# Kernel optimization log

Measured on AMD Instinct MI355X. Metric: run time of the kernel, lower is better.

## Reference

```python
import jax, jax.numpy as jnp
import numpy as np

DECAY = 0.99
LR = 0.01

def setup_inputs() -> dict:
    key = jax.random.key(0)
    ks = jax.random.split(key, 6)
    B, S, D, M = 4, 4096, 1024, 128
    sD = 1.0 / np.sqrt(D)
    sM = 1.0 / np.sqrt(M)
    return {
        "x": jax.random.normal(ks[0], (B, S, D), dtype=jnp.float32),
        "Wk": jax.random.uniform(ks[1], (M, D), jnp.float32, -sD, sD),
        "bk": jnp.zeros((M,), jnp.float32),
        "Wv": jax.random.uniform(ks[2], (M, D), jnp.float32, -sD, sD),
        "bv": jnp.zeros((M,), jnp.float32),
        "Wq": jax.random.uniform(ks[3], (M, D), jnp.float32, -sD, sD),
        "bq": jnp.zeros((M,), jnp.float32),
        "Wo": jax.random.uniform(ks[4], (D, M), jnp.float32, -sM, sM),
        "bo": jnp.zeros((D,), jnp.float32),
    }

def reference(x, Wk, bk, Wv, bv, Wq, bq, Wo, bo):
    B, S, D = x.shape
    M = Wk.shape[0]
    # Precompute all projections in one batched GEMM each: [B,S,M]
    k = jnp.einsum('bsd,md->bsm', x, Wk) + bk
    v = jnp.einsum('bsd,md->bsm', x, Wv) + bv
    q = jnp.einsum('bsd,md->bsm', x, Wq) + bq

    def step(state, kvq):
        k_t, v_t, q_t = kvq  # each [B, M]
        # readout uses the PRE-update state, matching the torch loop order
        out_t = jnp.einsum('bij,bj->bi', state, q_t)          # [B, M]
        state = DECAY * state + LR * jnp.einsum('bi,bj->bij', v_t, k_t)
        return state, out_t

    state0 = jnp.zeros((B, M, M), x.dtype)
    # scan over time: move seq axis to front -> [S, B, M]
    xs = (jnp.swapaxes(k, 0, 1), jnp.swapaxes(v, 0, 1), jnp.swapaxes(q, 0, 1))
    state, outs = jax.lax.scan(step, state0, xs)
    outs = jnp.swapaxes(outs, 0, 1)                            # [B, S, M]
    y = jnp.einsum('bsm,dm->bsd', outs, Wo) + bo               # [B, S, D]
    return (y, state)
```

## Files before the change

kernel.cpp:

```cpp
#include <hip/hip_runtime.h>
#include <math.h>

namespace {
constexpr int kB = 4;
constexpr int kS = 4096;
constexpr int kD = 1024;
constexpr int kM = 128;
constexpr int kC = 64;
constexpr int kNC = kS / kC;
constexpr int kNCG = kB * kNC;
constexpr int kRS = kB * kS;
constexpr float kLR = 0.01f;
constexpr float kLog2d = -0.0144995696f;
}

typedef __bf16 bf16x8 __attribute__((ext_vector_type(8)));
typedef float  f32x4  __attribute__((ext_vector_type(4)));
typedef unsigned short u16;
typedef unsigned int   u32;

#define SB0() __builtin_amdgcn_sched_barrier(0)
#define WAITV(N) asm volatile("s_waitcnt vmcnt(" #N ") lgkmcnt(0)" ::: "memory")

__device__ __forceinline__ u16 f2bf(float f) {
  u32 x = __float_as_uint(f);
  u32 r = (x + 0x7fffu + ((x >> 16) & 1u)) >> 16;
  return (u16)r;
}

__device__ __forceinline__ float bf2f(u16 h) {
  return __uint_as_float(((u32)h) << 16);
}

__device__ __forceinline__ void gl_lds16(const void* g, void* l) {
  __builtin_amdgcn_global_load_lds(
      (const __attribute__((address_space(1))) void*)g,
      (__attribute__((address_space(3))) void*)l, 16, 0, 0);
}

__device__ __forceinline__ f32x4 mf(bf16x8 a, bf16x8 b, f32x4 c) {
  return __builtin_amdgcn_mfma_f32_16x16x32_bf16(a, b, c, 0, 0, 0);
}

__device__ __forceinline__ ushort4 pack4(float4 a) {
  ushort4 o;
  o.x = f2bf(a.x); o.y = f2bf(a.y); o.z = f2bf(a.z); o.w = f2bf(a.w);
  return o;
}

__device__ __forceinline__ int fo64x128(int r, int c) {
  return ((r >> 4) * 4 + (c >> 5)) * 1024 + ((c >> 3) & 3) * 256 + (r & 15) * 16 + (c & 7) * 2;
}
__device__ __forceinline__ int fo128x64(int r, int c) {
  return ((r >> 4) * 2 + (c >> 5)) * 1024 + ((c >> 3) & 3) * 256 + (r & 15) * 16 + (c & 7) * 2;
}
__device__ __forceinline__ int fo64x64(int r, int c) {
  return ((r >> 4) * 2 + (c >> 5)) * 1024 + ((c >> 3) & 3) * 256 + (r & 15) * 16 + (c & 7) * 2;
}

__global__ __launch_bounds__(256)
void cast_w_kernel(const float* __restrict__ Wk, const float* __restrict__ Wv,
                   const float* __restrict__ Wq, const float* __restrict__ Wo,
                   u16* __restrict__ Wkvq, u16* __restrict__ Woh)
{
  int i = (blockIdx.x * 256 + threadIdx.x) * 4;
  const float* src;
  u16* dst;
  if (i < 393216) {
    src = (i < 131072) ? Wk + i : (i < 262144) ? Wv + (i - 131072) : Wq + (i - 262144);
    dst = Wkvq + i;
  } else {
    src = Wo + (i - 393216);
    dst = Woh + (i - 393216);
  }
  float4 v = *(const float4*)src;
  *(ushort4*)dst = pack4(v);
}

__global__ __launch_bounds__(256, 2)
void proj_gemm(const float* __restrict__ x, const u16* __restrict__ Wkvq,
               const float* __restrict__ bk, const float* __restrict__ bv,
               const float* __restrict__ bq,
               u16* __restrict__ Qg, u16* __restrict__ Kg,
               u16* __restrict__ VTg, u16* __restrict__ KwTg)
{
  __shared__ __align__(16) u16 L[36864];
  const int cg = blockIdx.x, s = blockIdx.y;
  const int R0 = cg * 64;
  const int tid = threadIdx.x, w = tid >> 6, lane = tid & 63;
  const int fr = lane & 15, qd = lane >> 4;
  const int wr = w >> 1, wc = w & 1;

  const int xr = tid >> 2, s4 = tid & 3;
  const float* xp = x + (size_t)(R0 + xr) * kD + s4 * 4;
  int aoffq[4];
#pragma unroll
  for (int q = 0; q < 4; ++q)
    aoffq[q] = ((xr >> 4) * 2 + (q >> 1)) * 1024 + (((s4 >> 1) + 2 * q) & 3) * 256
             + (xr & 15) * 16 + (s4 & 1) * 8;

  const u16* wbase = Wkvq + (size_t)(128 * s) * kD + qd * 8;

  f32x4 acc[2][4] = {};
  float4 xv0[4], xv1[4];

  auto compute = [&](int cs) {
    bf16x8 af[2][2], bfr2[2][4];
#pragma unroll
    for (int kh = 0; kh < 2; ++kh) {
#pragma unroll
      for (int mi = 0; mi < 2; ++mi)
        af[kh][mi] = *(const bf16x8*)&L[(cs * 8192 + ((wr * 2 + mi) * 2 + kh) * 1024 + qd * 256 + fr * 16) >> 1];
#pragma unroll
      for (int ng = 0; ng < 4; ++ng)
        bfr2[kh][ng] = *(const bf16x8*)&L[(24576 + cs * 16384 + ((wc * 4 + ng) * 2 + kh) * 1024 + qd * 256 + fr * 16) >> 1];
    }
#pragma unroll
    for (int kh = 0; kh < 2; ++kh)
#pragma unroll
      for (int mi = 0; mi < 2; ++mi)
#pragma unroll
        for (int ng = 0; ng < 4; ++ng)
          acc[mi][ng] = mf(af[kh][mi], bfr2[kh][ng], acc[mi][ng]);
  };

  auto step = [&](int t, float4 (&xw)[4], float4 (&xl)[4]) {
    const int wslot = (t + 1) % 3, ns = (t + 2) % 3;
#pragma unroll
    for (int q = 0; q < 4; ++q)
      *(ushort4*)&L[(wslot * 8192 + aoffq[q]) >> 1] = pack4(xw[q]);
    const int k2 = (t + 2) * 64;
#pragma unroll
    for (int g = 0; g < 4; ++g) {
      const int pn = 4 * w + g, ng = pn >> 1, kh = pn & 1;
      gl_lds16(wbase + (size_t)(ng * 16 + fr) * kD + k2 + kh * 32,
               &L[(24576 + ns * 16384 + pn * 1024) >> 1]);
    }
#pragma unroll
    for (int q = 0; q < 4; ++q) xl[q] = *(const float4*)(xp + k2 + q * 16);
    compute(t % 3);
    WAITV(8); SB0(); __builtin_amdgcn_s_barrier(); SB0();
  };

#pragma unroll
  for (int g = 0; g < 4; ++g) {
    const int pn = 4 * w + g, ng = pn >> 1, kh = pn & 1;
    gl_lds16(wbase + (size_t)(ng * 16 + fr) * kD + kh * 32, &L[(24576 + pn * 1024) >> 1]);
  }
#pragma unroll
  for (int q = 0; q < 4; ++q) xv0[q] = *(const float4*)(xp + q * 16);
#pragma unroll
  for (int q = 0; q < 4; ++q) *(ushort4*)&L[(0 + aoffq[q]) >> 1] = pack4(xv0[q]);
#pragma unroll
  for (int g = 0; g < 4; ++g) {
    const int pn = 4 * w + g, ng = pn >> 1, kh = pn & 1;
    gl_lds16(wbase + (size_t)(ng * 16 + fr) * kD + 64 + kh * 32,
             &L[(24576 + 16384 + pn * 1024) >> 1]);
  }
#pragma unroll
  for (int q = 0; q < 4; ++q) xv1[q] = *(const float4*)(xp + 64 + q * 16);
  WAITV(8); SB0(); __builtin_amdgcn_s_barrier(); SB0();

  for (int it = 0; it < 7; ++it) {
    step(2 * it, xv1, xv0);
    step(2 * it + 1, xv0, xv1);
  }
  {
#pragma unroll
    for (int q = 0; q < 4; ++q)
      *(ushort4*)&L[(0 + aoffq[q]) >> 1] = pack4(xv1[q]);
    compute(2);
    WAITV(0); SB0(); __builtin_amdgcn_s_barrier(); SB0();
  }
  compute(0);

  const float* bp = (s == 0) ? bk : (s == 1) ? bv : bq;
  float bias[4];
#pragma unroll
  for (int ng = 0; ng < 4; ++ng) bias[ng] = bp[wc * 64 + ng * 16 + fr];
  const size_t cb = (size_t)cg * 8192;

  if (s == 0) {
    float dp[2][4];
#pragma unroll
    for (int mi = 0; mi < 2; ++mi)
#pragma unroll
      for (int r = 0; r < 4; ++r)
        dp[mi][r] = kLR * exp2f((float)(63 - (wr * 32 + mi * 16 + qd * 4 + r)) * kLog2d);
#pragma unroll
    for (int mi = 0; mi < 2; ++mi)
#pragma unroll
      for (int ng = 0; ng < 4; ++ng)
#pragma unroll
        for (int r = 0; r < 4; ++r) {
          const int t = wr * 32 + mi * 16 + qd * 4 + r, n = wc * 64 + ng * 16 + fr;
          const float v = acc[mi][ng][r] + bias[ng];
          Kg[cb + (fo64x128(t, n) >> 1)] = f2bf(v);
          KwTg[cb + (fo128x64(n, t) >> 1)] = f2bf(v * dp[mi][r]);
        }
  } else if (s == 1) {
#pragma unroll
    for (int mi = 0; mi < 2; ++mi)
#pragma unroll
      for (int ng = 0; ng < 4; ++ng)
#pragma unroll
        for (int r = 0; r < 4; ++r) {
          const int t = wr * 32 + mi * 16 + qd * 4 + r, n = wc * 64 + ng * 16 + fr;
          VTg[cb + (fo128x64(n, t) >> 1)] = f2bf(acc[mi][ng][r] + bias[ng]);
        }
  } else {
#pragma unroll
    for (int mi = 0; mi < 2; ++mi)
#pragma unroll
      for (int ng = 0; ng < 4; ++ng)
#pragma unroll
        for (int r = 0; r < 4; ++r) {
          const int t = wr * 32 + mi * 16 + qd * 4 + r, n = wc * 64 + ng * 16 + fr;
          Qg[cb + (fo64x128(t, n) >> 1)] = f2bf(acc[mi][ng][r] + bias[ng]);
        }
  }
}

__global__ __launch_bounds__(256, 2)
void intra_kernel(const u16* __restrict__ Qg, const u16* __restrict__ Kg,
                  const u16* __restrict__ VTg, const u16* __restrict__ KwTg,
                  u16* __restrict__ O1g, float* __restrict__ SU)
{
  __shared__ __align__(16) u16 L[32768];
  const int cg = blockIdx.x;
  const int tid = threadIdx.x, w = tid >> 6, lane = tid & 63;
  const int fr = lane & 15, qd = lane >> 4;
  const size_t cb = (size_t)cg * 8192;

#pragma unroll
  for (int g = 0; g < 4; ++g) {
    const int pn = 4 * w + g;
    gl_lds16(Qg + cb + pn * 512 + lane * 8, &L[(0 + pn * 1024) >> 1]);
    gl_lds16(Kg + cb + pn * 512 + lane * 8, &L[(16384 + pn * 1024) >> 1]);
    gl_lds16(VTg + cb + pn * 512 + lane * 8, &L[(32768 + pn * 1024) >> 1]);
    gl_lds16(KwTg + cb + pn * 512 + lane * 8, &L[(49152 + pn * 1024) >> 1]);
  }
  __syncthreads();

  f32x4 p[4] = {};
#pragma unroll
  for (int kc = 0; kc < 4; ++kc) {
    bf16x8 aq = *(const bf16x8*)&L[(0 + (w * 4 + kc) * 1024 + qd * 256 + fr * 16) >> 1];
#pragma unroll
    for (int ug = 0; ug < 4; ++ug) {
      bf16x8 bkf = *(const bf16x8*)&L[(16384 + (ug * 4 + kc) * 1024 + qd * 256 + fr * 16) >> 1];
      p[ug] = mf(aq, bkf, p[ug]);
    }
  }
  __syncthreads();

#pragma unroll
  for (int ug = 0; ug < 4; ++ug)
#pragma unroll
    for (int r = 0; r < 4; ++r) {
      const int t = w * 16 + qd * 4 + r, u = ug * 16 + fr;
      float av = 0.f;
      if (u < t) av = kLR * exp2f((float)(t - 1 - u) * kLog2d) * p[ug][r];
      L[(0 + fo64x64(t, u)) >> 1] = f2bf(av);
    }
  __syncthreads();

  f32x4 o1[8] = {}, uu[2][8] = {};
#pragma unroll
  for (int h = 0; h < 2; ++h) {
    bf16x8 aA = *(const bf16x8*)&L[(0 + (w * 2 + h) * 1024 + qd * 256 + fr * 16) >> 1];
    bf16x8 aV[2];
#pragma unroll
    for (int mi = 0; mi < 2; ++mi)
      aV[mi] = *(const bf16x8*)&L[(32768 + ((2 * w + mi) * 2 + h) * 1024 + qd * 256 + fr * 16) >> 1];
#pragma unroll
    for (int ig = 0; ig < 8; ++ig) {
      bf16x8 bV = *(const bf16x8*)&L[(32768 + (ig * 2 + h) * 1024 + qd * 256 + fr * 16) >> 1];
      o1[ig] = mf(aA, bV, o1[ig]);
    }
#pragma unroll
    for (int jg = 0; jg < 8; ++jg) {
      bf16x8 bK = *(const bf16x8*)&L[(49152 + (jg * 2 + h) * 1024 + qd * 256 + fr * 16) >> 1];
#pragma unroll
      for (int mi = 0; mi < 2; ++mi)
        uu[mi][jg] = mf(aV[mi], bK, uu[mi][jg]);
    }
  }

#pragma unroll
  for (int ig = 0; ig < 8; ++ig)
#pragma unroll
    for (int r = 0; r < 4; ++r) {
      const int t = w * 16 + qd * 4 + r, i2 = ig * 16 + fr;
      O1g[cb + (fo64x128(t, i2) >> 1)] = f2bf(o1[ig][r]);
    }
  float* SUc = SU + (size_t)cg * 16384;
#pragma unroll
  for (int mi = 0; mi < 2; ++mi)
#pragma unroll
    for (int jg = 0; jg < 8; ++jg)
#pragma unroll
      for (int r = 0; r < 4; ++r) {
        const int i2 = w * 32 + mi * 16 + qd * 4 + r, j = jg * 16 + fr;
        SUc[i2 * kM + j] = uu[mi][jg][r];
      }
}

__global__ __launch_bounds__(256)
void scan_kernel(const float* __restrict__ SU, u16* __restrict__ Sb16,
                 float* __restrict__ state_out)
{
  const int e = blockIdx.x * 256 + threadIdx.x;
  const int b = e >> 14, ij = e & 16383;
  const float* base = SU + (size_t)b * kNC * 16384 + ij;
  u16* sb = Sb16 + (size_t)b * kNC * 16384 + ij;
  const float dC = exp2f((float)kC * kLog2d);
  float prev = 0.f;
#pragma unroll 8
  for (int c2 = 0; c2 < kNC; ++c2) {
    const float u = base[(size_t)c2 * 16384];
    sb[(size_t)c2 * 16384] = f2bf(prev);
    prev = fmaf(dC, prev, u);
  }
  state_out[e] = prev;
}

__global__ __launch_bounds__(256)
void fused_combine_out(const u16* __restrict__ Qg, const u16* __restrict__ Sb16,
                       const u16* __restrict__ O1g, const u16* __restrict__ Woh,
                       const float* __restrict__ bo, float* __restrict__ y)
{
  __shared__ __align__(16) u16 L[32768];
  const int cg = blockIdx.x;
  const int R0 = cg * 64;
  const int tid = threadIdx.x, w = tid >> 6, lane = tid & 63;
  const int fr = lane & 15, qd = lane >> 4;
  const size_t cb = (size_t)cg * 8192;
  const u16* Sbc = Sb16 + (size_t)cg * 16384;

#pragma unroll
  for (int g = 0; g < 4; ++g) {
    const int pn = 4 * w + g;
    gl_lds16(Qg + cb + pn * 512 + lane * 8, &L[(0 + pn * 1024) >> 1]);
    gl_lds16(O1g + cb + pn * 512 + lane * 8, &L[(49152 + pn * 1024) >> 1]);
  }
#pragma unroll
  for (int g = 0; g < 8; ++g) {
    const int pn = 8 * w + g, ig = pn >> 2, kc = pn & 3;
    gl_lds16(Sbc + (size_t)(ig * 16 + fr) * kM + kc * 32 + qd * 8,
             &L[(16384 + pn * 1024) >> 1]);
  }
  __syncthreads();

  f32x4 o2[8] = {};
#pragma unroll
  for (int kc = 0; kc < 4; ++kc) {
    bf16x8 aq = *(const bf16x8*)&L[(0 + (w * 4 + kc) * 1024 + qd * 256 + fr * 16) >> 1];
#pragma unroll
    for (int ig = 0; ig < 8; ++ig) {
      bf16x8 bS = *(const bf16x8*)&L[(16384 + (ig * 4 + kc) * 1024 + qd * 256 + fr * 16) >> 1];
      o2[ig] = mf(aq, bS, o2[ig]);
    }
  }

  float dt[4];
#pragma unroll
  for (int r = 0; r < 4; ++r) dt[r] = exp2f((float)(w * 16 + qd * 4 + r) * kLog2d);
#pragma unroll
  for (int ig = 0; ig < 8; ++ig)
#pragma unroll
    for (int r = 0; r < 4; ++r) {
      const int t = w * 16 + qd * 4 + r, i2 = ig * 16 + fr;
      const float o1v = bf2f(L[(49152 + fo64x128(t, i2)) >> 1]);
      L[(0 + fo64x128(t, i2)) >> 1] = f2bf(fmaf(dt[r], o2[ig][r], o1v));
    }
  __syncthreads();

#pragma unroll 1
  for (int h = 0; h < 2; ++h) {
    const int n0 = w * 256 + h * 128;
    f32x4 fy[4][8] = {};
#pragma unroll
    for (int kp = 0; kp < 4; ++kp) {
      bf16x8 ao[4], bw[8];
#pragma unroll
      for (int mi = 0; mi < 4; ++mi)
        ao[mi] = *(const bf16x8*)&L[((mi * 4 + kp) * 1024 + qd * 256 + fr * 16) >> 1];
#pragma unroll
      for (int nj = 0; nj < 8; ++nj)
        bw[nj] = *(const bf16x8*)&Woh[(size_t)(n0 + nj * 16 + fr) * kM + kp * 32 + qd * 8];
#pragma unroll
      for (int mi = 0; mi < 4; ++mi)
#pragma unroll
        for (int nj = 0; nj < 8; ++nj)
          fy[mi][nj] = mf(ao[mi], bw[nj], fy[mi][nj]);
    }
#pragma unroll
    for (int nj = 0; nj < 8; ++nj) {
      const int d = n0 + nj * 16 + fr;
      const float bb = bo[d];
#pragma unroll
      for (int mi = 0; mi < 4; ++mi)
#pragma unroll
        for (int r = 0; r < 4; ++r)
          y[(size_t)(R0 + mi * 16 + qd * 4 + r) * kD + d] = fy[mi][nj][r] + bb;
    }
  }
}

extern "C" void kernel_launch(void* const* d_in, const int* in_sizes, int n_in,
                              void* d_out, int out_size, void* d_ws, size_t ws_size,
                              hipStream_t stream) {
  const float* x  = (const float*)d_in[0];
  const float* Wk = (const float*)d_in[1];
  const float* bk = (const float*)d_in[2];
  const float* Wv = (const float*)d_in[3];
  const float* bv = (const float*)d_in[4];
  const float* Wq = (const float*)d_in[5];
  const float* bq = (const float*)d_in[6];
  const float* Wo = (const float*)d_in[7];
  const float* bo = (const float*)d_in[8];

  char* wsp = (char*)d_ws;
  u16* Wkvq = (u16*)wsp;  wsp += (size_t)384 * 1024 * 2;
  u16* Woh  = (u16*)wsp;  wsp += (size_t)1024 * 128 * 2;
  u16* Qg   = (u16*)wsp;  wsp += (size_t)kNCG * 8192 * 2;
  u16* Kg   = (u16*)wsp;  wsp += (size_t)kNCG * 8192 * 2;
  u16* VTg  = (u16*)wsp;
  u16* KwTg = VTg + (size_t)kNCG * 8192;
  u16* Sb16 = VTg;
  wsp += (size_t)kNCG * 16384 * 2;
  u16* O1g  = (u16*)wsp;  wsp += (size_t)kNCG * 8192 * 2;
  float* SU = (float*)wsp; wsp += (size_t)kNCG * 16384 * 4;

  float* y = (float*)d_out;
  float* state_out = y + (size_t)kRS * kD;

  cast_w_kernel<<<dim3(512), dim3(256), 0, stream>>>(Wk, Wv, Wq, Wo, Wkvq, Woh);
  proj_gemm<<<dim3(kNCG, 3), dim3(256), 0, stream>>>(x, Wkvq, bk, bv, bq, Qg, Kg, VTg, KwTg);
  intra_kernel<<<dim3(kNCG), dim3(256), 0, stream>>>(Qg, Kg, VTg, KwTg, O1g, SU);
  scan_kernel<<<dim3(kB * 16384 / 256), dim3(256), 0, stream>>>(SU, Sb16, state_out);
  fused_combine_out<<<dim3(kNCG), dim3(256), 0, stream>>>(Qg, Sb16, O1g, Woh, bo, y);
}
```

Before: 195.3 us.

## Fuse K/V/Q projection GEMM with intra-chunk attention in one kernel

Merges proj_gemm and intra_kernel into a single 512-thread kernel. Each block computes all three projections for a 64-row chunk, loading x straight into registers as MFMA A fragments instead of staging it through LDS. K, V^T, Kw^T and Q are then kept in LDS for the intra-chunk products, so only Q goes to global memory. This removes a launch and the global round trip for K, V and Kw, but the grid drops from 768 to 256 blocks, which may hurt occupancy and latency hiding.

```diff
diff --git a/kernel.cpp b/kernel.cpp
--- a/kernel.cpp
+++ b/kernel.cpp
@@ -46,6 +46,13 @@
   ushort4 o;
   o.x = f2bf(a.x); o.y = f2bf(a.y); o.z = f2bf(a.z); o.w = f2bf(a.w);
   return o;
+}
+
+__device__ __forceinline__ bf16x8 packbf(float4 a, float4 b) {
+  union { u16 h[8]; bf16x8 v; } r;
+  r.h[0] = f2bf(a.x); r.h[1] = f2bf(a.y); r.h[2] = f2bf(a.z); r.h[3] = f2bf(a.w);
+  r.h[4] = f2bf(b.x); r.h[5] = f2bf(b.y); r.h[6] = f2bf(b.z); r.h[7] = f2bf(b.w);
+  return r.v;
 }
 
 __device__ __forceinline__ int fo64x128(int r, int c) {
@@ -77,233 +84,169 @@
   *(ushort4*)dst = pack4(v);
 }
 
-__global__ __launch_bounds__(256, 2)
-void proj_gemm(const float* __restrict__ x, const u16* __restrict__ Wkvq,
-               const float* __restrict__ bk, const float* __restrict__ bv,
-               const float* __restrict__ bq,
-               u16* __restrict__ Qg, u16* __restrict__ Kg,
-               u16* __restrict__ VTg, u16* __restrict__ KwTg)
+__global__ __launch_bounds__(512)
+void proj_intra(const float* __restrict__ x, const u16* __restrict__ Wkvq,
+                const float* __restrict__ bk, const float* __restrict__ bv,
+                const float* __restrict__ bq,
+                u16* __restrict__ Qg, u16* __restrict__ O1g,
+                float* __restrict__ SU)
 {
-  __shared__ __align__(16) u16 L[36864];
-  const int cg = blockIdx.x, s = blockIdx.y;
+  __shared__ __align__(16) u16 L[49152];
+  const int cg = blockIdx.x;
   const int R0 = cg * 64;
   const int tid = threadIdx.x, w = tid >> 6, lane = tid & 63;
   const int fr = lane & 15, qd = lane >> 4;
-  const int wr = w >> 1, wc = w & 1;
-
-  const int xr = tid >> 2, s4 = tid & 3;
-  const float* xp = x + (size_t)(R0 + xr) * kD + s4 * 4;
-  int aoffq[4];
-#pragma unroll
-  for (int q = 0; q < 4; ++q)
-    aoffq[q] = ((xr >> 4) * 2 + (q >> 1)) * 1024 + (((s4 >> 1) + 2 * q) & 3) * 256
-             + (xr & 15) * 16 + (s4 & 1) * 8;
-
-  const u16* wbase = Wkvq + (size_t)(128 * s) * kD + qd * 8;
-
-  f32x4 acc[2][4] = {};
-  float4 xv0[4], xv1[4];
-
-  auto compute = [&](int cs) {
-    bf16x8 af[2][2], bfr2[2][4];
-#pragma unroll
-    for (int kh = 0; kh < 2; ++kh) {
-#pragma unroll
-      for (int mi = 0; mi < 2; ++mi)
-        af[kh][mi] = *(const bf16x8*)&L[(cs * 8192 + ((wr * 2 + mi) * 2 + kh) * 1024 + qd * 256 + fr * 16) >> 1];
-#pragma unroll
-      for (int ng = 0; ng < 4; ++ng)
-        bfr2[kh][ng] = *(const bf16x8*)&L[(24576 + cs * 16384 + ((wc * 4 + ng) * 2 + kh) * 1024 + qd * 256 + fr * 16) >> 1];
-    }
-#pragma unroll
-    for (int kh = 0; kh < 2; ++kh)
-#pragma unroll
-      for (int mi = 0; mi < 2; ++mi)
-#pragma unroll
-        for (int ng = 0; ng < 4; ++ng)
-          acc[mi][ng] = mf(af[kh][mi], bfr2[kh][ng], acc[mi][ng]);
+  const int rw = w & 3, cw = w >> 2;
+
+  constexpr int Bs0 = 0, Bs1 = 49152;
+  constexpr int QsB = 0, KsB = 16384, VTB = 32768, KwB = 49152;
+
+  const int p0 = 6 * w;
+  const float* xrow = x + (size_t)(R0 + rw * 16 + fr) * kD + qd * 8;
+  const size_t cb = (size_t)cg * 8192;
+
+  f32x4 acc[12] = {};
+  float4 xA0, xB0, xA1, xB1;
+  float4 yA0, yB0, yA1, yB1;
+
+  auto stageB = [&](int t, int buf) {
+    const int k0 = t * 64;
+#pragma unroll
+    for (int j = 0; j < 6; ++j) {
+      const int p = p0 + j;
+      gl_lds16(Wkvq + (size_t)((p >> 1) * 16 + fr) * kD + k0 + (p & 1) * 32 + qd * 8,
+               &L[(buf + p * 1024) >> 1]);
+    }
   };
-
-  auto step = [&](int t, float4 (&xw)[4], float4 (&xl)[4]) {
-    const int wslot = (t + 1) % 3, ns = (t + 2) % 3;
-#pragma unroll
-    for (int q = 0; q < 4; ++q)
-      *(ushort4*)&L[(wslot * 8192 + aoffq[q]) >> 1] = pack4(xw[q]);
-    const int k2 = (t + 2) * 64;
-#pragma unroll
-    for (int g = 0; g < 4; ++g) {
-      const int pn = 4 * w + g, ng = pn >> 1, kh = pn & 1;
-      gl_lds16(wbase + (size_t)(ng * 16 + fr) * kD + k2 + kh * 32,
-               &L[(24576 + ns * 16384 + pn * 1024) >> 1]);
-    }
-#pragma unroll
-    for (int q = 0; q < 4; ++q) xl[q] = *(const float4*)(xp + k2 + q * 16);
-    compute(t % 3);
-    WAITV(8); SB0(); __builtin_amdgcn_s_barrier(); SB0();
+  auto loadA = [&](int t, float4& A0, float4& B0, float4& A1, float4& B1) {
+    const int k0 = t * 64;
+    A0 = *(const float4*)(xrow + k0);
+    B0 = *(const float4*)(xrow + k0 + 4);
+    A1 = *(const float4*)(xrow + k0 + 32);
+    B1 = *(const float4*)(xrow + k0 + 36);
   };
-
-#pragma unroll
-  for (int g = 0; g < 4; ++g) {
-    const int pn = 4 * w + g, ng = pn >> 1, kh = pn & 1;
-    gl_lds16(wbase + (size_t)(ng * 16 + fr) * kD + kh * 32, &L[(24576 + pn * 1024) >> 1]);
-  }
-#pragma unroll
-  for (int q = 0; q < 4; ++q) xv0[q] = *(const float4*)(xp + q * 16);
-#pragma unroll
-  for (int q = 0; q < 4; ++q) *(ushort4*)&L[(0 + aoffq[q]) >> 1] = pack4(xv0[q]);
-#pragma unroll
-  for (int g = 0; g < 4; ++g) {
-    const int pn = 4 * w + g, ng = pn >> 1, kh = pn & 1;
-    gl_lds16(wbase + (size_t)(ng * 16 + fr) * kD + 64 + kh * 32,
-             &L[(24576 + 16384 + pn * 1024) >> 1]);
-  }
-#pragma unroll
-  for (int q = 0; q < 4; ++q) xv1[q] = *(const float4*)(xp + 64 + q * 16);
-  WAITV(8); SB0(); __builtin_amdgcn_s_barrier(); SB0();
+  auto computeStep = [&](int buf, const float4& A0, const float4& B0,
+                         const float4& A1, const float4& B1) {
+    bf16x8 a[2];
+    a[0] = packbf(A0, B0);
+    a[1] = packbf(A1, B1);
+#pragma unroll
+    for (int kc = 0; kc < 2; ++kc)
+#pragma unroll
+      for (int nf = 0; nf < 12; ++nf) {
+        const int p = (cw * 12 + nf) * 2 + kc;
+        bf16x8 b = *(const bf16x8*)&L[(buf + p * 1024 + qd * 256 + fr * 16) >> 1];
+        acc[nf] = mf(a[kc], b, acc[nf]);
+      }
+  };
+
+  stageB(0, Bs0);
+  loadA(0, xA0, xB0, xA1, xB1);
+  WAITV(4); SB0(); __builtin_amdgcn_s_barrier(); SB0();
 
   for (int it = 0; it < 7; ++it) {
-    step(2 * it, xv1, xv0);
-    step(2 * it + 1, xv0, xv1);
-  }
-  {
-#pragma unroll
-    for (int q = 0; q < 4; ++q)
-      *(ushort4*)&L[(0 + aoffq[q]) >> 1] = pack4(xv1[q]);
-    compute(2);
-    WAITV(0); SB0(); __builtin_amdgcn_s_barrier(); SB0();
-  }
-  compute(0);
-
-  const float* bp = (s == 0) ? bk : (s == 1) ? bv : bq;
-  float bias[4];
-#pragma unroll
-  for (int ng = 0; ng < 4; ++ng) bias[ng] = bp[wc * 64 + ng * 16 + fr];
-  const size_t cb = (size_t)cg * 8192;
-
-  if (s == 0) {
-    float dp[2][4];
-#pragma unroll
-    for (int mi = 0; mi < 2; ++mi)
-#pragma unroll
-      for (int r = 0; r < 4; ++r)
-        dp[mi][r] = kLR * exp2f((float)(63 - (wr * 32 + mi * 16 + qd * 4 + r)) * kLog2d);
-#pragma unroll
-    for (int mi = 0; mi < 2; ++mi)
-#pragma unroll
-      for (int ng = 0; ng < 4; ++ng)
-#pragma unroll
-        for (int r = 0; r < 4; ++r) {
-          const int t = wr * 32 + mi * 16 + qd * 4 + r, n = wc * 64 + ng * 16 + fr;
-          const float v = acc[mi][ng][r] + bias[ng];
-          Kg[cb + (fo64x128(t, n) >> 1)] = f2bf(v);
-          KwTg[cb + (fo128x64(n, t) >> 1)] = f2bf(v * dp[mi][r]);
-        }
-  } else if (s == 1) {
-#pragma unroll
-    for (int mi = 0; mi < 2; ++mi)
-#pragma unroll
-      for (int ng = 0; ng < 4; ++ng)
-#pragma unroll
-        for (int r = 0; r < 4; ++r) {
-          const int t = wr * 32 + mi * 16 + qd * 4 + r, n = wc * 64 + ng * 16 + fr;
-          VTg[cb + (fo128x64(n, t) >> 1)] = f2bf(acc[mi][ng][r] + bias[ng]);
-        }
-  } else {
-#pragma unroll
-    for (int mi = 0; mi < 2; ++mi)
-#pragma unroll
-      for (int ng = 0; ng < 4; ++ng)
-#pragma unroll
-        for (int r = 0; r < 4; ++r) {
-          const int t = wr * 32 + mi * 16 + qd * 4 + r, n = wc * 64 + ng * 16 + fr;
-          Qg[cb + (fo64x128(t, n) >> 1)] = f2bf(acc[mi][ng][r] + bias[ng]);
-        }
-  }
-}
-
-__global__ __launch_bounds__(256, 2)
-void intra_kernel(const u16* __restrict__ Qg, const u16* __restrict__ Kg,
-                  const u16* __restrict__ VTg, const u16* __restrict__ KwTg,
-                  u16* __restrict__ O1g, float* __restrict__ SU)
-{
-  __shared__ __align__(16) u16 L[32768];
-  const int cg = blockIdx.x;
-  const int tid = threadIdx.x, w = tid >> 6, lane = tid & 63;
-  const int fr = lane & 15, qd = lane >> 4;
-  const size_t cb = (size_t)cg * 8192;
-
-#pragma unroll
-  for (int g = 0; g < 4; ++g) {
-    const int pn = 4 * w + g;
-    gl_lds16(Qg + cb + pn * 512 + lane * 8, &L[(0 + pn * 1024) >> 1]);
-    gl_lds16(Kg + cb + pn * 512 + lane * 8, &L[(16384 + pn * 1024) >> 1]);
-    gl_lds16(VTg + cb + pn * 512 + lane * 8, &L[(32768 + pn * 1024) >> 1]);
-    gl_lds16(KwTg + cb + pn * 512 + lane * 8, &L[(49152 + pn * 1024) >> 1]);
-  }
-  __syncthreads();
-
-  f32x4 p[4] = {};
+    const int te = 2 * it;
+    stageB(te + 1, Bs1); loadA(te + 1, yA0, yB0, yA1, yB1);
+    computeStep(Bs0, xA0, xB0, xA1, xB1);
+    WAITV(4); SB0(); __builtin_amdgcn_s_barrier(); SB0();
+    stageB(te + 2, Bs0); loadA(te + 2, xA0, xB0, xA1, xB1);
+    computeStep(Bs1, yA0, yB0, yA1, yB1);
+    WAITV(4); SB0(); __builtin_amdgcn_s_barrier(); SB0();
+  }
+  stageB(15, Bs1); loadA(15, yA0, yB0, yA1, yB1);
+  computeStep(Bs0, xA0, xB0, xA1, xB1);
+  WAITV(4); SB0(); __builtin_amdgcn_s_barrier(); SB0();
+  computeStep(Bs1, yA0, yB0, yA1, yB1);
+  __syncthreads();
+
+  float dp[4];
+#pragma unroll
+  for (int r = 0; r < 4; ++r)
+    dp[r] = kLR * exp2f((float)(63 - (rw * 16 + qd * 4 + r)) * kLog2d);
+
+#pragma unroll
+  for (int nf = 0; nf < 12; ++nf) {
+    const int g = cw * 12 + nf;
+    const int slab = g >> 3;
+    const int jj = (g & 7) * 16 + fr;
+    const float* bp = (slab == 0) ? bk : (slab == 1) ? bv : bq;
+    const float bias = bp[jj];
+#pragma unroll
+    for (int r = 0; r < 4; ++r) {
+      const int t = rw * 16 + qd * 4 + r;
+      const float val = acc[nf][r] + bias;
+      const u16 h = f2bf(val);
+      if (slab == 0) {
+        L[(KsB + fo64x128(t, jj)) >> 1] = h;
+        L[(KwB + fo128x64(jj, t)) >> 1] = f2bf(val * dp[r]);
+      } else if (slab == 1) {
+        L[(VTB + fo128x64(jj, t)) >> 1] = h;
+      } else {
+        L[(QsB + fo64x128(t, jj)) >> 1] = h;
+        Qg[cb + (fo64x128(t, jj) >> 1)] = h;
+      }
+    }
+  }
+  __syncthreads();
+
+  const int tf = w >> 1, uf0 = (w & 1) * 2;
+  f32x4 p2[2] = {};
 #pragma unroll
   for (int kc = 0; kc < 4; ++kc) {
-    bf16x8 aq = *(const bf16x8*)&L[(0 + (w * 4 + kc) * 1024 + qd * 256 + fr * 16) >> 1];
-#pragma unroll
-    for (int ug = 0; ug < 4; ++ug) {
-      bf16x8 bkf = *(const bf16x8*)&L[(16384 + (ug * 4 + kc) * 1024 + qd * 256 + fr * 16) >> 1];
-      p[ug] = mf(aq, bkf, p[ug]);
-    }
-  }
-  __syncthreads();
-
-#pragma unroll
-  for (int ug = 0; ug < 4; ++ug)
-#pragma unroll
-    for (int r = 0; r < 4; ++r) {
-      const int t = w * 16 + qd * 4 + r, u = ug * 16 + fr;
+    bf16x8 aq = *(const bf16x8*)&L[(QsB + (tf * 4 + kc) * 1024 + qd * 256 + fr * 16) >> 1];
+#pragma unroll
+    for (int ui = 0; ui < 2; ++ui) {
+      bf16x8 bkf = *(const bf16x8*)&L[(KsB + ((uf0 + ui) * 4 + kc) * 1024 + qd * 256 + fr * 16) >> 1];
+      p2[ui] = mf(aq, bkf, p2[ui]);
+    }
+  }
+  __syncthreads();
+
+#pragma unroll
+  for (int ui = 0; ui < 2; ++ui)
+#pragma unroll
+    for (int r = 0; r < 4; ++r) {
+      const int t = tf * 16 + qd * 4 + r;
+      const int u = (uf0 + ui) * 16 + fr;
       float av = 0.f;
-      if (u < t) av = kLR * exp2f((float)(t - 1 - u) * kLog2d) * p[ug][r];
-      L[(0 + fo64x64(t, u)) >> 1] = f2bf(av);
-    }
-  __syncthreads();
-
-  f32x4 o1[8] = {}, uu[2][8] = {};
-#pragma unroll
-  for (int h = 0; h < 2; ++h) {
-    bf16x8 aA = *(const bf16x8*)&L[(0 + (w * 2 + h) * 1024 + qd * 256 + fr * 16) >> 1];
-    bf16x8 aV[2];
-#pragma unroll
-    for (int mi = 0; mi < 2; ++mi)
-      aV[mi] = *(const bf16x8*)&L[(32768 + ((2 * w + mi) * 2 + h) * 1024 + qd * 256 + fr * 16) >> 1];
-#pragma unroll
-    for (int ig = 0; ig < 8; ++ig) {
-      bf16x8 bV = *(const bf16x8*)&L[(32768 + (ig * 2 + h) * 1024 + qd * 256 + fr * 16) >> 1];
-      o1[ig] = mf(aA, bV, o1[ig]);
-    }
-#pragma unroll
-    for (int jg = 0; jg < 8; ++jg) {
-      bf16x8 bK = *(const bf16x8*)&L[(49152 + (jg * 2 + h) * 1024 + qd * 256 + fr * 16) >> 1];
-#pragma unroll
-      for (int mi = 0; mi < 2; ++mi)
-        uu[mi][jg] = mf(aV[mi], bK, uu[mi][jg]);
-    }
-  }
-
-#pragma unroll
-  for (int ig = 0; ig < 8; ++ig)
-#pragma unroll
-    for (int r = 0; r < 4; ++r) {
-      const int t = w * 16 + qd * 4 + r, i2 = ig * 16 + fr;
-      O1g[cb + (fo64x128(t, i2) >> 1)] = f2bf(o1[ig][r]);
+      if (u < t) av = kLR * exp2f((float)(t - 1 - u) * kLog2d) * p2[ui][r];
+      L[(KsB + fo64x64(t, u)) >> 1] = f2bf(av);
+    }
+  __syncthreads();
+
+  const int ih = w & 1;
+  f32x4 o1[4] = {}, uu[8] = {};
+#pragma unroll
+  for (int kc = 0; kc < 2; ++kc) {
+    bf16x8 aA = *(const bf16x8*)&L[(KsB + (tf * 2 + kc) * 1024 + qd * 256 + fr * 16) >> 1];
+    bf16x8 aV = *(const bf16x8*)&L[(VTB + (w * 2 + kc) * 1024 + qd * 256 + fr * 16) >> 1];
+#pragma unroll
+    for (int ni = 0; ni < 4; ++ni) {
+      bf16x8 bV = *(const bf16x8*)&L[(VTB + ((ih * 4 + ni) * 2 + kc) * 1024 + qd * 256 + fr * 16) >> 1];
+      o1[ni] = mf(aA, bV, o1[ni]);
+    }
+#pragma unroll
+    for (int jf = 0; jf < 8; ++jf) {
+      bf16x8 bK = *(const bf16x8*)&L[(KwB + (jf * 2 + kc) * 1024 + qd * 256 + fr * 16) >> 1];
+      uu[jf] = mf(aV, bK, uu[jf]);
+    }
+  }
+
+#pragma unroll
+  for (int ni = 0; ni < 4; ++ni)
+#pragma unroll
+    for (int r = 0; r < 4; ++r) {
+      const int t = tf * 16 + qd * 4 + r, i2 = (ih * 4 + ni) * 16 + fr;
+      O1g[cb + (fo64x128(t, i2) >> 1)] = f2bf(o1[ni][r]);
     }
   float* SUc = SU + (size_t)cg * 16384;
 #pragma unroll
-  for (int mi = 0; mi < 2; ++mi)
-#pragma unroll
-    for (int jg = 0; jg < 8; ++jg)
-#pragma unroll
-      for (int r = 0; r < 4; ++r) {
-        const int i2 = w * 32 + mi * 16 + qd * 4 + r, j = jg * 16 + fr;
-        SUc[i2 * kM + j] = uu[mi][jg][r];
-      }
+  for (int jf = 0; jf < 8; ++jf)
+#pragma unroll
+    for (int r = 0; r < 4; ++r) {
+      const int i2 = w * 16 + qd * 4 + r, j = jf * 16 + fr;
+      SUc[i2 * kM + j] = uu[jf][r];
+    }
 }
 
 __global__ __launch_bounds__(256)
@@ -422,23 +365,18 @@
   const float* bo = (const float*)d_in[8];
 
   char* wsp = (char*)d_ws;
-  u16* Wkvq = (u16*)wsp;  wsp += (size_t)384 * 1024 * 2;
-  u16* Woh  = (u16*)wsp;  wsp += (size_t)1024 * 128 * 2;
-  u16* Qg   = (u16*)wsp;  wsp += (size_t)kNCG * 8192 * 2;
-  u16* Kg   = (u16*)wsp;  wsp += (size_t)kNCG * 8192 * 2;
-  u16* VTg  = (u16*)wsp;
-  u16* KwTg = VTg + (size_t)kNCG * 8192;
-  u16* Sb16 = VTg;
-  wsp += (size_t)kNCG * 16384 * 2;
-  u16* O1g  = (u16*)wsp;  wsp += (size_t)kNCG * 8192 * 2;
+  u16* Wkvq = (u16*)wsp;   wsp += (size_t)384 * 1024 * 2;
+  u16* Woh  = (u16*)wsp;   wsp += (size_t)1024 * 128 * 2;
+  u16* Qg   = (u16*)wsp;   wsp += (size_t)kNCG * 8192 * 2;
+  u16* O1g  = (u16*)wsp;   wsp += (size_t)kNCG * 8192 * 2;
+  u16* Sb16 = (u16*)wsp;   wsp += (size_t)kNCG * 16384 * 2;
   float* SU = (float*)wsp; wsp += (size_t)kNCG * 16384 * 4;
 
   float* y = (float*)d_out;
   float* state_out = y + (size_t)kRS * kD;
 
   cast_w_kernel<<<dim3(512), dim3(256), 0, stream>>>(Wk, Wv, Wq, Wo, Wkvq, Woh);
-  proj_gemm<<<dim3(kNCG, 3), dim3(256), 0, stream>>>(x, Wkvq, bk, bv, bq, Qg, Kg, VTg, KwTg);
-  intra_kernel<<<dim3(kNCG), dim3(256), 0, stream>>>(Qg, Kg, VTg, KwTg, O1g, SU);
+  proj_intra<<<dim3(kNCG), dim3(512), 0, stream>>>(x, Wkvq, bk, bv, bq, Qg, O1g, SU);
   scan_kernel<<<dim3(kB * 16384 / 256), dim3(256), 0, stream>>>(SU, Sb16, state_out);
   fused_combine_out<<<dim3(kNCG), dim3(256), 0, stream>>>(Qg, Sb16, O1g, Woh, bo, y);
 }
```

After: 190.4 us. 2.5% less time.
